# Kernel tuning notes

Hardware: AMD Instinct MI355X
Metric: run time of the kernel (lower is better)

The kernel has to match this reference:

```python
import jax, jax.numpy as jnp
import numpy as np

_SAMPLING_EPS = 1e-5


def setup_inputs() -> dict:
    key = jax.random.key(0)
    ks = jax.random.split(key, 7)
    N, V, H = 256, 128000, 200  # num_seqs, vocab_size, output-history length
    logits = jax.random.normal(ks[0], (N, V), dtype=jnp.float32)
    output_tokens = jax.random.randint(ks[1], (N, H), 0, V, dtype=jnp.int32)
    presence_penalties = jax.random.uniform(ks[2], (N,), jnp.float32, 0.0, 2.0)
    frequency_penalties = jax.random.uniform(ks[3], (N,), jnp.float32, 0.0, 2.0)
    temperatures = jax.random.uniform(ks[4], (N,), jnp.float32, 0.5, 1.5)
    top_ps = jax.random.uniform(ks[5], (N,), jnp.float32, 0.5, 1.0)
    top_ks = jax.random.randint(ks[6], (N,), 1, 1000, dtype=jnp.int32)
    return {
        "logits": logits,
        "presence_penalties": presence_penalties,
        "frequency_penalties": frequency_penalties,
        "temperatures": temperatures,
        "top_ps": top_ps,
        "output_tokens": output_tokens,
        "top_ks": top_ks,
    }


def reference(logits, presence_penalties, frequency_penalties, temperatures,
              top_ps, output_tokens, top_ks):
    N, V = logits.shape

    # ---- _apply_penalties: bincount of previously generated tokens per row ----
    rows = jnp.arange(N)[:, None]  # [N,1] broadcast against [N,H] token ids
    bin_counts = jnp.zeros((N, V), logits.dtype).at[rows, output_tokens].add(1.0)
    # rows are skipped when both penalties are < eps (original builds an index list)
    active = ((presence_penalties >= _SAMPLING_EPS) |
              (frequency_penalties >= _SAMPLING_EPS))[:, None]
    presence_mask = (bin_counts > 0.0).astype(logits.dtype)
    penalty = (frequency_penalties[:, None] * bin_counts
               + presence_penalties[:, None] * presence_mask)
    logits = logits - jnp.where(active, penalty, jnp.zeros((), logits.dtype))

    # ---- temperature scaling + softmax ----
    logits = logits / temperatures[:, None]
    probs = jax.nn.softmax(logits, axis=-1)

    # ---- _apply_top_p_top_k: sort desc, cumsum, mask, unsort ----
    probs_idx = jnp.argsort(-probs, axis=-1)                    # descending order
    probs_sort = jnp.take_along_axis(probs, probs_idx, axis=-1)
    probs_sum = jnp.cumsum(probs_sort, axis=-1)
    top_p_mask = (probs_sum - probs_sort) > top_ps[:, None]     # exclusive cumsum > p
    probs_sort = jnp.where(top_p_mask, 0.0, probs_sort)
    top_k_mask = jnp.arange(V, dtype=top_ks.dtype)[None, :] >= top_ks[:, None]
    probs_sort = jnp.where(top_k_mask, 0.0, probs_sort)
    inv_idx = jnp.argsort(probs_idx, axis=-1)                   # unsort permutation
    filtered_probs = jnp.take_along_axis(probs_sort, inv_idx, axis=-1)
    return filtered_probs
```

## Files before the change

### kernel.cpp

```cpp
#include <hip/hip_runtime.h>
#include <stdint.h>

#define NB 8192
#define BSHIFT 19
#define HS 512
#define HM 511
#define CAP 4096
#define PCAP 2048
#define NRB 2048
#define NT 1024

typedef unsigned long long ull;

__device__ __forceinline__ unsigned mono_u32(float x) {
    unsigned b = __float_as_uint(x);
    return (b & 0x80000000u) ? ~b : (b | 0x80000000u);
}
__device__ __forceinline__ float inv_mono(unsigned u) {
    unsigned b = (u & 0x80000000u) ? (u & 0x7fffffffu) : ~u;
    return __uint_as_float(b);
}

__device__ __forceinline__ float compute_x(float l, int cnt,
                                           float pres, float freq, float t) {
    float pen = __fadd_rn(__fmul_rn(freq, (float)cnt), (cnt > 0) ? pres : 0.0f);
    return __fdiv_rn(__fsub_rn(l, pen), t);
}

__global__ __launch_bounds__(NT) void k_fused(
    const float* __restrict__ logits, const int* __restrict__ tokens,
    const float* __restrict__ pres_v, const float* __restrict__ freq_v,
    const float* __restrict__ temps, const float* __restrict__ topp_v,
    const int* __restrict__ topk_v, int V, int H, float* __restrict__ out)
{
    __shared__ __align__(16) char smem[(32 + 16 + 8 + 4) * 1024];
    unsigned* hc = (unsigned*)smem;
    ull* skey = (ull*)smem;
    char* regB = smem + 32 * 1024;
    float* se = (float*)regB;
    int* sct = (int*)regB;
    int* sct2 = (int*)(regB + 4 * 1024);
    ull* tmpc = (ull*)regB;
    char* regC = smem + 48 * 1024;
    float* bs1 = (float*)regC;
    float* bs2 = (float*)(regC + 4 * 1024);
    unsigned* rh = (unsigned*)regC;
    char* regD = smem + 56 * 1024;
    int* hkey = (int*)regD;
    int* hval = (int*)(regD + 2 * 1024);
    __shared__ float esum_s, corr_s;
    __shared__ int bstar_s, lcnt_s, rb_s, pcnt_s;

    int row = blockIdx.x, tid = threadIdx.x;
    for (int b = tid; b < NB; b += NT) hc[b] = 0u;
    if (tid == 0) { esum_s = 0.f; corr_s = 0.f; bstar_s = -1; lcnt_s = 0; rb_s = 0; pcnt_s = 0; }

    for (int i = tid; i < HS; i += NT) { hkey[i] = -1; hval[i] = 0; }
    __syncthreads();
    const int* trow = tokens + (size_t)row * H;
    for (int i = tid; i < H; i += NT) {
        int v = trow[i];
        unsigned h = ((unsigned)v * 2654435761u) >> 23;
        while (true) {
            int prev = atomicCAS(&hkey[h], -1, v);
            if (prev == -1 || prev == v) { atomicAdd(&hval[h], 1); break; }
            h = (h + 1) & HM;
        }
    }
    __syncthreads();

    float t = temps[row];
    float r = __fdiv_rn(1.0f, t);
    const float* lrow = logits + (size_t)row * V;
    const float4* l4p = (const float4*)lrow;
    int V4 = V >> 2;

    float es = 0.0f;
    int i = tid;
    for (; i + 7 * NT < V4; i += 8 * NT) {
        float4 arr[8];
#pragma unroll
        for (int q = 0; q < 8; ++q) arr[q] = l4p[i + q * NT];
#pragma unroll
        for (int q = 0; q < 8; ++q)
#pragma unroll
            for (int j = 0; j < 4; ++j) {
                float x = __fmul_rn((&arr[q].x)[j], r);
                atomicAdd(&hc[mono_u32(x) >> BSHIFT], 1u);
                es += __expf(x);
            }
    }
    for (; i < V4; i += NT) {
        float4 A = l4p[i];
#pragma unroll
        for (int j = 0; j < 4; ++j) {
            float x = __fmul_rn((&A.x)[j], r);
            atomicAdd(&hc[mono_u32(x) >> BSHIFT], 1u);
            es += __expf(x);
        }
    }
    for (int v = (V4 << 2) + tid; v < V; v += NT) {
        float x = __fmul_rn(lrow[v], r);
        atomicAdd(&hc[mono_u32(x) >> BSHIFT], 1u);
        es += __expf(x);
    }
    for (int off = 32; off; off >>= 1) es += __shfl_down(es, off);
    if ((tid & 63) == 0) atomicAdd(&esum_s, es);
    __syncthreads();

    float pres = pres_v[row], freq = freq_v[row];
    int active = (pres >= 1e-5f) || (freq >= 1e-5f);
    float corr = 0.0f;
    if (active) {
        for (int s = tid; s < HS; s += NT) {
            int v = hkey[s];
            if (v >= 0) {
                int c = hval[s];
                float l = lrow[v];
                float x0 = __fmul_rn(l, r);
                float xp = compute_x(l, c, pres, freq, t);
                unsigned b0 = mono_u32(x0) >> BSHIFT;
                unsigned bp = mono_u32(xp) >> BSHIFT;
                if (b0 != bp) { atomicSub(&hc[b0], 1u); atomicAdd(&hc[bp], 1u); }
                corr += __expf(xp) - __expf(x0);
            }
        }
    }
    for (int off = 32; off; off >>= 1) corr += __shfl_down(corr, off);
    if ((tid & 63) == 0) atomicAdd(&corr_s, corr);
    __syncthreads();

    const int BPT = NB / NT;
    int base = tid * BPT;
    int acc = 0;
#pragma unroll
    for (int q = BPT - 1; q >= 0; --q) { acc += (int)hc[base + q]; hc[base + q] = (unsigned)acc; }
    sct[tid] = acc;
    __syncthreads();
    {
        int* a = sct; int* b2 = sct2;
        for (int s = 1; s < NT; s <<= 1) {
            int v = a[tid] + ((tid + s < NT) ? a[tid + s] : 0);
            __syncthreads();
            b2[tid] = v;
            __syncthreads();
            int* tmp = a; a = b2; b2 = tmp;
        }
        int above = (tid < NT - 1) ? a[tid + 1] : 0;
        int k = topk_v[row];
        int best = -1;
#pragma unroll
        for (int q = BPT - 1; q >= 0; --q)
            if ((int)hc[base + q] + above >= k) { best = base + q; break; }
        if (best >= 0) atomicMax(&bstar_s, best);
    }
    __syncthreads();
    int bst = bstar_s - 2;
    if (bst < 0) bst = 0;
    float Sp = esum_s + corr_s;
    __syncthreads();

    float4* o4p = (float4*)(out + (size_t)row * V);
    const float4 z4 = make_float4(0.f, 0.f, 0.f, 0.f);
    i = tid;
    for (; i + 7 * NT < V4; i += 8 * NT) {
        float4 arr[8];
#pragma unroll
        for (int q = 0; q < 8; ++q) arr[q] = l4p[i + q * NT];
#pragma unroll
        for (int q = 0; q < 8; ++q) o4p[i + q * NT] = z4;
#pragma unroll
        for (int q = 0; q < 8; ++q) {
            int vb = (i + q * NT) << 2;
#pragma unroll
            for (int j = 0; j < 4; ++j) {
                float l = (&arr[q].x)[j];
                unsigned ua = mono_u32(__fmul_rn(l, r));
                if ((int)(ua >> BSHIFT) >= bst) {
                    unsigned ue = mono_u32(__fdiv_rn(l, t));
                    int pos = atomicAdd(&lcnt_s, 1);
                    if (pos < CAP)
                        skey[pos] = ((ull)ue << 32) | (unsigned)~(unsigned)(vb + j);
                }
            }
        }
    }
    for (; i < V4; i += NT) {
        float4 A = l4p[i];
        o4p[i] = z4;
#pragma unroll
        for (int j = 0; j < 4; ++j) {
            float l = (&A.x)[j];
            unsigned ua = mono_u32(__fmul_rn(l, r));
            if ((int)(ua >> BSHIFT) >= bst) {
                unsigned ue = mono_u32(__fdiv_rn(l, t));
                int pos = atomicAdd(&lcnt_s, 1);
                if (pos < CAP)
                    skey[pos] = ((ull)ue << 32) | (unsigned)~(unsigned)((i << 2) + j);
            }
        }
    }
    for (int v = (V4 << 2) + tid; v < V; v += NT) {
        float l = lrow[v];
        out[(size_t)row * V + v] = 0.0f;
        unsigned ua = mono_u32(__fmul_rn(l, r));
        if ((int)(ua >> BSHIFT) >= bst) {
            unsigned ue = mono_u32(__fdiv_rn(l, t));
            int pos = atomicAdd(&lcnt_s, 1);
            if (pos < CAP)
                skey[pos] = ((ull)ue << 32) | (unsigned)~(unsigned)v;
        }
    }
    __syncthreads();
    int count = lcnt_s; if (count > CAP) count = CAP;
    int k = topk_v[row];

    if (active) {
        for (int j = tid; j < count; j += NT) {
            unsigned idx = ~(unsigned)(skey[j] & 0xffffffffull);
            unsigned h = (idx * 2654435761u) >> 23;
            int c = 0;
            while (true) {
                int kk = hkey[h];
                if (kk == (int)idx) { c = hval[h]; break; }
                if (kk == -1) break;
                h = (h + 1) & HM;
            }
            if (c > 0) {
                float xp = compute_x(lrow[idx], c, pres, freq, t);
                skey[j] = ((ull)mono_u32(xp) << 32) | (unsigned)~idx;
            }
        }
    }
    __syncthreads();
    for (int g = tid; g < NRB; g += NT) rh[g] = 0u;
    __syncthreads();
    int gmin = bst << 6;
    for (int j = tid; j < count; j += NT) {
        unsigned u = (unsigned)(skey[j] >> 32);
        int rel = (int)(u >> 13) - gmin;
        rel = rel < 0 ? 0 : (rel > NRB - 1 ? NRB - 1 : rel);
        atomicAdd(&rh[rel], 1u);
    }
    __syncthreads();
    {
        int b2i = tid * 2;
        int a2 = (int)rh[b2i + 1];
        rh[b2i + 1] = (unsigned)a2;
        a2 += (int)rh[b2i];
        rh[b2i] = (unsigned)a2;
        sct[tid] = a2;
        __syncthreads();
        int* a = sct; int* b2 = sct2;
        for (int s = 1; s < NT; s <<= 1) {
            int v = a[tid] + ((tid + s < NT) ? a[tid + s] : 0);
            __syncthreads();
            b2[tid] = v;
            __syncthreads();
            int* tmp = a; a = b2; b2 = tmp;
        }
        int above = (tid < NT - 1) ? a[tid + 1] : 0;
        int best = -1;
        if ((int)rh[b2i + 1] + above >= k) best = b2i + 1;
        else if ((int)rh[b2i] + above >= k) best = b2i;
        if (best >= 0) atomicMax(&rb_s, best);
    }
    __syncthreads();
    int rb = rb_s;
    for (int j = tid; j < count; j += NT) {
        unsigned u = (unsigned)(skey[j] >> 32);
        int rel = (int)(u >> 13) - gmin;
        rel = rel < 0 ? 0 : (rel > NRB - 1 ? NRB - 1 : rel);
        if (rel >= rb) {
            int pos = atomicAdd(&pcnt_s, 1);
            if (pos < PCAP) tmpc[pos] = skey[j];
        }
    }
    __syncthreads();
    int count2 = pcnt_s;
    if (count2 <= PCAP) {
        for (int j = tid; j < count2; j += NT) skey[j] = tmpc[j];
        count = count2;
    }
    __syncthreads();

    int m = 1; while (m < count) m <<= 1;
    for (int j = count + tid; j < m; j += NT) skey[j] = 0ull;
    __syncthreads();
    for (int kk = 2; kk <= m; kk <<= 1) {
        for (int jj = kk >> 1; jj > 0; jj >>= 1) {
            for (int i2 = tid; i2 < m; i2 += NT) {
                int ixj = i2 ^ jj;
                if (ixj > i2) {
                    ull A = skey[i2], B = skey[ixj];
                    bool up = ((i2 & kk) != 0);
                    if ((A > B) == up) { skey[i2] = B; skey[ixj] = A; }
                }
            }
            __syncthreads();
        }
    }

    for (int j = tid; j < CAP; j += NT)
        se[j] = (j < count) ? __expf(inv_mono((unsigned)(skey[j] >> 32))) : 0.0f;
    __syncthreads();
    int j0 = tid << 2;
    float e0 = se[j0], e1 = se[j0 + 1], e2 = se[j0 + 2], e3 = se[j0 + 3];
    float c0 = e0, c1 = c0 + e1, c2 = c1 + e2, c3 = c2 + e3;
    bs1[tid] = c3;
    __syncthreads();
    float* a = bs1; float* b2 = bs2;
    for (int s = 1; s < NT; s <<= 1) {
        float v = a[tid] + ((tid >= s) ? a[tid - s] : 0.0f);
        __syncthreads();
        b2[tid] = v;
        __syncthreads();
        float* tmp = a; a = b2; b2 = tmp;
    }
    float pre = (tid > 0) ? a[tid - 1] : 0.0f;

    float pS = topp_v[row] * Sp;
    float inc[4] = {pre + c0, pre + c1, pre + c2, pre + c3};
    float ee[4] = {e0, e1, e2, e3};
#pragma unroll
    for (int q = 0; q < 4; ++q) {
        int j = j0 + q;
        if (j < count) {
            float e = ee[q];
            float excl = __fsub_rn(inc[q], e);
            if ((j < k) && (excl <= pS)) {
                unsigned idx = ~(unsigned)(skey[j] & 0xffffffffull);
                out[(size_t)row * V + idx] = __fdiv_rn(e, Sp);
            }
        }
    }
}

extern "C" void kernel_launch(void* const* d_in, const int* in_sizes, int n_in,
                              void* d_out, int out_size, void* d_ws, size_t ws_size,
                              hipStream_t stream) {
    const float* logits = (const float*)d_in[0];
    const float* pres   = (const float*)d_in[1];
    const float* freq   = (const float*)d_in[2];
    const float* temps  = (const float*)d_in[3];
    const float* topps  = (const float*)d_in[4];
    const int*   tokens = (const int*)d_in[5];
    const int*   topks  = (const int*)d_in[6];
    int N = in_sizes[1];
    int V = in_sizes[0] / N;
    int H = in_sizes[5] / N;
    float* out = (float*)d_out;

    k_fused<<<N, NT, 0, stream>>>(logits, tokens, pres, freq, temps, topps,
                                  topks, V, H, out);
}
```

Baseline: 291.9 us.

## Replace block-wide Hillis-Steele scans with wavefront shuffle scans; zero output in first pass

Swaps the three shared-memory Hillis-Steele scans, each needing about 20 barriers, for wavefront shuffle scans plus a small per-wave total array that takes one barrier. Zeroing of the output row moves from the second logits pass into the first, so the stores overlap the histogram/exp pass. This cuts barrier latency in the single-block-per-row kernel. Float prefix-sum order changes slightly, which can perturb top-p boundary decisions.

```diff
diff --git a/kernel.cpp b/kernel.cpp
--- a/kernel.cpp
+++ b/kernel.cpp
@@ -38,20 +38,19 @@
     ull* skey = (ull*)smem;
     char* regB = smem + 32 * 1024;
     float* se = (float*)regB;
-    int* sct = (int*)regB;
-    int* sct2 = (int*)(regB + 4 * 1024);
     ull* tmpc = (ull*)regB;
     char* regC = smem + 48 * 1024;
-    float* bs1 = (float*)regC;
-    float* bs2 = (float*)(regC + 4 * 1024);
     unsigned* rh = (unsigned*)regC;
     char* regD = smem + 56 * 1024;
     int* hkey = (int*)regD;
     int* hval = (int*)(regD + 2 * 1024);
+    __shared__ int wt_i[16];
+    __shared__ float wt_f[16];
     __shared__ float esum_s, corr_s;
     __shared__ int bstar_s, lcnt_s, rb_s, pcnt_s;
 
     int row = blockIdx.x, tid = threadIdx.x;
+    int lane = tid & 63, wid = tid >> 6;
     for (int b = tid; b < NB; b += NT) hc[b] = 0u;
     if (tid == 0) { esum_s = 0.f; corr_s = 0.f; bstar_s = -1; lcnt_s = 0; rb_s = 0; pcnt_s = 0; }
 
@@ -73,6 +72,8 @@
     float r = __fdiv_rn(1.0f, t);
     const float* lrow = logits + (size_t)row * V;
     const float4* l4p = (const float4*)lrow;
+    float4* o4p = (float4*)(out + (size_t)row * V);
+    const float4 z4 = make_float4(0.f, 0.f, 0.f, 0.f);
     int V4 = V >> 2;
 
     float es = 0.0f;
@@ -82,6 +83,8 @@
 #pragma unroll
         for (int q = 0; q < 8; ++q) arr[q] = l4p[i + q * NT];
 #pragma unroll
+        for (int q = 0; q < 8; ++q) o4p[i + q * NT] = z4;
+#pragma unroll
         for (int q = 0; q < 8; ++q)
 #pragma unroll
             for (int j = 0; j < 4; ++j) {
@@ -92,6 +95,7 @@
     }
     for (; i < V4; i += NT) {
         float4 A = l4p[i];
+        o4p[i] = z4;
 #pragma unroll
         for (int j = 0; j < 4; ++j) {
             float x = __fmul_rn((&A.x)[j], r);
@@ -101,6 +105,7 @@
     }
     for (int v = (V4 << 2) + tid; v < V; v += NT) {
         float x = __fmul_rn(lrow[v], r);
+        out[(size_t)row * V + v] = 0.0f;
         atomicAdd(&hc[mono_u32(x) >> BSHIFT], 1u);
         es += __expf(x);
     }
@@ -135,19 +140,19 @@
     int acc = 0;
 #pragma unroll
     for (int q = BPT - 1; q >= 0; --q) { acc += (int)hc[base + q]; hc[base + q] = (unsigned)acc; }
-    sct[tid] = acc;
-    __syncthreads();
+    int k = topk_v[row];
     {
-        int* a = sct; int* b2 = sct2;
-        for (int s = 1; s < NT; s <<= 1) {
-            int v = a[tid] + ((tid + s < NT) ? a[tid + s] : 0);
-            __syncthreads();
-            b2[tid] = v;
-            __syncthreads();
-            int* tmp = a; a = b2; b2 = tmp;
-        }
-        int above = (tid < NT - 1) ? a[tid + 1] : 0;
-        int k = topk_v[row];
+        int v = acc;
+#pragma unroll
+        for (int off = 1; off < 64; off <<= 1) {
+            int o = __shfl_down(v, off);
+            if (lane + off < 64) v += o;
+        }
+        if (lane == 0) wt_i[wid] = v;
+        __syncthreads();
+        int above = v - acc;
+#pragma unroll
+        for (int w = 0; w < 16; ++w) if (w > wid) above += wt_i[w];
         int best = -1;
 #pragma unroll
         for (int q = BPT - 1; q >= 0; --q)
@@ -160,15 +165,11 @@
     float Sp = esum_s + corr_s;
     __syncthreads();
 
-    float4* o4p = (float4*)(out + (size_t)row * V);
-    const float4 z4 = make_float4(0.f, 0.f, 0.f, 0.f);
     i = tid;
     for (; i + 7 * NT < V4; i += 8 * NT) {
         float4 arr[8];
 #pragma unroll
         for (int q = 0; q < 8; ++q) arr[q] = l4p[i + q * NT];
-#pragma unroll
-        for (int q = 0; q < 8; ++q) o4p[i + q * NT] = z4;
 #pragma unroll
         for (int q = 0; q < 8; ++q) {
             int vb = (i + q * NT) << 2;
@@ -187,7 +188,6 @@
     }
     for (; i < V4; i += NT) {
         float4 A = l4p[i];
-        o4p[i] = z4;
 #pragma unroll
         for (int j = 0; j < 4; ++j) {
             float l = (&A.x)[j];
@@ -202,7 +202,6 @@
     }
     for (int v = (V4 << 2) + tid; v < V; v += NT) {
         float l = lrow[v];
-        out[(size_t)row * V + v] = 0.0f;
         unsigned ua = mono_u32(__fmul_rn(l, r));
         if ((int)(ua >> BSHIFT) >= bst) {
             unsigned ue = mono_u32(__fdiv_rn(l, t));
@@ -213,7 +212,6 @@
     }
     __syncthreads();
     int count = lcnt_s; if (count > CAP) count = CAP;
-    int k = topk_v[row];
 
     if (active) {
         for (int j = tid; j < count; j += NT) {
@@ -249,17 +247,17 @@
         rh[b2i + 1] = (unsigned)a2;
         a2 += (int)rh[b2i];
         rh[b2i] = (unsigned)a2;
-        sct[tid] = a2;
+        int v = a2;
+#pragma unroll
+        for (int off = 1; off < 64; off <<= 1) {
+            int o = __shfl_down(v, off);
+            if (lane + off < 64) v += o;
+        }
+        if (lane == 0) wt_i[wid] = v;
         __syncthreads();
-        int* a = sct; int* b2 = sct2;
-        for (int s = 1; s < NT; s <<= 1) {
-            int v = a[tid] + ((tid + s < NT) ? a[tid + s] : 0);
-            __syncthreads();
-            b2[tid] = v;
-            __syncthreads();
-            int* tmp = a; a = b2; b2 = tmp;
-        }
-        int above = (tid < NT - 1) ? a[tid + 1] : 0;
+        int above = v - a2;
+#pragma unroll
+        for (int w = 0; w < 16; ++w) if (w > wid) above += wt_i[w];
         int best = -1;
         if ((int)rh[b2i + 1] + above >= k) best = b2i + 1;
         else if ((int)rh[b2i] + above >= k) best = b2i;
@@ -307,17 +305,17 @@
     int j0 = tid << 2;
     float e0 = se[j0], e1 = se[j0 + 1], e2 = se[j0 + 2], e3 = se[j0 + 3];
     float c0 = e0, c1 = c0 + e1, c2 = c1 + e2, c3 = c2 + e3;
-    bs1[tid] = c3;
-    __syncthreads();
-    float* a = bs1; float* b2 = bs2;
-    for (int s = 1; s < NT; s <<= 1) {
-        float v = a[tid] + ((tid >= s) ? a[tid - s] : 0.0f);
-        __syncthreads();
-        b2[tid] = v;
-        __syncthreads();
-        float* tmp = a; a = b2; b2 = tmp;
-    }
-    float pre = (tid > 0) ? a[tid - 1] : 0.0f;
+    float vf = c3;
+#pragma unroll
+    for (int off = 1; off < 64; off <<= 1) {
+        float o = __shfl_up(vf, off);
+        if (lane >= off) vf += o;
+    }
+    if (lane == 63) wt_f[wid] = vf;
+    __syncthreads();
+    float pre = vf - c3;
+#pragma unroll
+    for (int w = 0; w < 16; ++w) if (w < wid) pre += wt_f[w];
 
     float pS = topp_v[row] * Sp;
     float inc[4] = {pre + c0, pre + c1, pre + c2, pre + c3};
```

New measurement: 308.8 us. 5.8% more time.
